# Kernel tuning notes

Measured on AMD Instinct MI355X. Metric: run time of the kernel, lower is better.

Reference implementation:

```python
import jax, jax.numpy as jnp
import numpy as np

H = 1024        # pegasus-large hidden size
HEADS = 16      # matches the hard-coded /16 in the source
T = 512         # decoder steps
N = 1024        # encoder (source) tokens
V = 96103       # pegasus tokenizer vocab size


def setup_inputs() -> dict:
    key = jax.random.key(0)
    ks = jax.random.split(key, 8)
    return {
        "cross_attn": jax.random.normal(ks[0], (1, HEADS, T, N), jnp.float32),
        "encoder_hidden": jax.random.normal(ks[1], (1, N, H), jnp.float32),
        "decoder_hidden": jax.random.normal(ks[2], (1, T, H), jnp.float32),
        "decoder_embedding": jax.random.normal(ks[3], (1, T, H), jnp.float32),
        "logits": jax.random.normal(ks[4], (1, T, V), jnp.float32),
        "input_ids": jax.random.randint(ks[5], (N,), 0, V),
        "pointer_w": jax.random.normal(ks[6], (1, 3 * H), jnp.float32) * 0.02,
        "pointer_b": jnp.zeros((1,), jnp.float32),
    }


def reference(cross_attn, encoder_hidden, decoder_hidden, decoder_embedding,
              logits, input_ids, pointer_w, pointer_b):
    # squeeze batch dim (module assumes batch=1)
    ca = jnp.sum(cross_attn[0], axis=0) / 16.0                 # [T, N] head-avg cross attn
    enc = encoder_hidden[0]                                    # [N, H]
    dec_h = decoder_hidden[0]                                  # [T, H]
    dec_e = decoder_embedding[0]                               # [T, H]
    lg = logits[0]                                             # [T, V]

    h = ca @ enc                                               # [T, H] attn-weighted context
    lin = jnp.concatenate([h, dec_h, dec_e], axis=1)           # [T, 3H]
    gen_probs = jax.nn.sigmoid(lin @ pointer_w.T + pointer_b)  # [T, 1]

    distribution = jax.nn.softmax(lg, axis=1)                  # [T, V]
    gen_logits = gen_probs * distribution                      # [T, V]

    # vectorized form of: for t, for n: copy_logits[t, input_ids[n]] = ca[t, n]
    Tn, Vn = lg.shape
    rows = jnp.broadcast_to(jnp.arange(Tn)[:, None], ca.shape)       # [T, N]
    cols = jnp.broadcast_to(input_ids[None, :], ca.shape)            # [T, N]
    copy_logits = jnp.zeros((Tn, Vn), lg.dtype).at[rows, cols].set(ca)

    final_probs = gen_logits + (1.0 - gen_probs) * copy_logits  # [T, V]
    return gen_probs, final_probs
```

## Files before the change

kernel.cpp:

```cpp
#include <hip/hip_runtime.h>

#define Tn 512
#define Nn 1024
#define Hn 1024
#define Vn 96103u
#define NHEADS 16
#define SPLITS 16
#define CHUNK 6007u
#define TV 49204736u

#define HS_BLKS 512
#define EW_BLKS 1024
#define SP_BLKS (SPLITS*Tn)
#define K0_BLKS (HS_BLKS + EW_BLKS + SP_BLKS)

typedef float f4 __attribute__((ext_vector_type(4)));

__device__ __forceinline__ unsigned enc1(float x) {
  unsigned u = __float_as_uint(x);
  u = u + 0x80000u + ((u >> 20) & 1u);
  return (u >> 20) - 896u;
}
__device__ __forceinline__ float dec1(unsigned w, int k) {
  unsigned byte = (w >> (8 * k)) & 0xFFu;
  return __uint_as_float((byte + 896u) << 20);
}

__global__ __launch_bounds__(256) void k0(const float* __restrict__ attn,
                                          const float* __restrict__ enc,
                                          const float* __restrict__ w,
                                          const float* __restrict__ lg,
                                          float* __restrict__ ca,
                                          float* __restrict__ ew,
                                          float* __restrict__ part_s,
                                          int* __restrict__ col2n,
                                          unsigned char* __restrict__ ebuf) {
  const int b = blockIdx.x, tid = threadIdx.x;

  if (b < HS_BLKS) {
    int i = b * 256 + tid;
    if (i < (int)Vn) col2n[i] = -1;
    const f4* a4 = (const f4*)attn;
    const int slice = (Tn * Nn) / 4;
    f4 acc = __builtin_nontemporal_load(&a4[i]);
#pragma unroll
    for (int h = 1; h < NHEADS; ++h)
      acc += __builtin_nontemporal_load(&a4[h * slice + i]);
    ((f4*)ca)[i] = acc * (1.0f / 16.0f);
    return;
  }

  if (b < HS_BLKS + EW_BLKS) {
    int n = b - HS_BLKS;
    float4 r = ((const float4*)(enc + n * Hn))[tid];
    float4 ww = ((const float4*)w)[tid];
    float p = r.x * ww.x + r.y * ww.y + r.z * ww.z + r.w * ww.w;
    for (int off = 32; off > 0; off >>= 1) p += __shfl_down(p, off, 64);
    __shared__ float lds[4];
    int lane = tid & 63, wv = tid >> 6;
    if (lane == 0) lds[wv] = p;
    __syncthreads();
    if (tid == 0) ew[n] = lds[0] + lds[1] + lds[2] + lds[3];
    return;
  }

  {
    int rem = b - HS_BLKS - EW_BLKS;
    const int c = rem & (SPLITS - 1), t = rem >> 4;
    const unsigned vbeg = (unsigned)c * CHUNK;
    const unsigned vend = min(vbeg + CHUNK, Vn);
    const unsigned beg = (unsigned)t * Vn + vbeg;
    const unsigned end = (unsigned)t * Vn + vend;
    const unsigned beg4 = (beg + 3u) & ~3u;
    const unsigned end4 = end & ~3u;

    float s = 0.0f;
    for (unsigned i = beg + tid; i < beg4; i += 256) {
      float e = __expf(__builtin_nontemporal_load(&lg[i]));
      s += e; ebuf[i] = (unsigned char)enc1(e);
    }
    const f4* lg4 = (const f4*)lg;
    unsigned* eb4 = (unsigned*)ebuf;
    for (unsigned i4 = beg4 / 4u + tid; i4 < end4 / 4u; i4 += 256) {
      f4 a = __builtin_nontemporal_load(&lg4[i4]);
      float e0 = __expf(a[0]), e1 = __expf(a[1]), e2 = __expf(a[2]), e3 = __expf(a[3]);
      s += (e0 + e1) + (e2 + e3);
      eb4[i4] = enc1(e0) | (enc1(e1) << 8) | (enc1(e2) << 16) | (enc1(e3) << 24);
    }
    for (unsigned i = end4 + tid; i < end; i += 256) {
      float e = __expf(__builtin_nontemporal_load(&lg[i]));
      s += e; ebuf[i] = (unsigned char)enc1(e);
    }
    for (int off = 32; off > 0; off >>= 1) s += __shfl_down(s, off, 64);
    __shared__ float ls[4];
    int lane = tid & 63, wv = tid >> 6;
    if (lane == 0) ls[wv] = s;
    __syncthreads();
    if (tid == 0) part_s[t * SPLITS + c] = ls[0] + ls[1] + ls[2] + ls[3];
  }
}

__global__ __launch_bounds__(256) void k1(const float* __restrict__ ca,
                                          const float* __restrict__ ew,
                                          const float* __restrict__ dh,
                                          const float* __restrict__ de,
                                          const float* __restrict__ w,
                                          const float* __restrict__ b,
                                          const float* __restrict__ part_s,
                                          const int* __restrict__ ids,
                                          int* __restrict__ col2n,
                                          float4* __restrict__ params,
                                          float* __restrict__ out_gen) {
  const int t = blockIdx.x, tid = threadIdx.x;
  if (t == Tn) {
    for (int n = tid; n < (int)Nn; n += 256)
      atomicMax(&col2n[ids[n]], n);
    return;
  }
  float4 c4 = ((const float4*)(ca + t * Nn))[tid];
  float4 e4 = ((const float4*)ew)[tid];
  float p = c4.x * e4.x + c4.y * e4.y + c4.z * e4.z + c4.w * e4.w;
  float4 h4 = ((const float4*)(dh + t * Hn))[tid];
  float4 w1 = ((const float4*)(w + Hn))[tid];
  p += h4.x * w1.x + h4.y * w1.y + h4.z * w1.z + h4.w * w1.w;
  float4 d4 = ((const float4*)(de + t * Hn))[tid];
  float4 w2 = ((const float4*)(w + 2 * Hn))[tid];
  p += d4.x * w2.x + d4.y * w2.y + d4.z * w2.z + d4.w * w2.w;
  for (int off = 32; off > 0; off >>= 1) p += __shfl_down(p, off, 64);
  __shared__ float lds[4];
  int lane = tid & 63, wv = tid >> 6;
  if (lane == 0) lds[wv] = p;
  __syncthreads();
  if (tid == 0) {
    float z = lds[0] + lds[1] + lds[2] + lds[3] + b[0];
    float g = 1.0f / (1.0f + __expf(-z));
    float S = 0.0f;
#pragma unroll
    for (int c = 0; c < SPLITS; ++c) S += part_s[t * SPLITS + c];
    out_gen[t] = g;
    params[t] = make_float4(g, 1.0f / S, 1.0f - g, 0.0f);
  }
}

__global__ __launch_bounds__(256) void k2(const unsigned* __restrict__ eb4,
                                          const float* __restrict__ ca,
                                          const float4* __restrict__ params,
                                          const int* __restrict__ col2n,
                                          float* __restrict__ out) {
  const unsigned total4 = TV / 4u;
  f4* out4 = (f4*)out;
  const unsigned stride = gridDim.x * 256u;
  for (unsigned i4 = blockIdx.x * 256u + threadIdx.x; i4 < total4; i4 += stride) {
    unsigned i0 = i4 * 4u;
    unsigned t = i0 / Vn;
    unsigned v = i0 - t * Vn;
    unsigned dw = eb4[i4];
    f4 r;
    if (v + 3u < Vn) {
      float4 P = params[t];
      const float* cat = ca + t * Nn;
      int n0 = col2n[v], n1 = col2n[v + 1], n2 = col2n[v + 2], n3 = col2n[v + 3];
      r[0] = P.x * dec1(dw, 0) * P.y;
      r[1] = P.x * dec1(dw, 1) * P.y;
      r[2] = P.x * dec1(dw, 2) * P.y;
      r[3] = P.x * dec1(dw, 3) * P.y;
      if (n0 >= 0) r[0] += P.z * cat[n0];
      if (n1 >= 0) r[1] += P.z * cat[n1];
      if (n2 >= 0) r[2] += P.z * cat[n2];
      if (n3 >= 0) r[3] += P.z * cat[n3];
    } else {
#pragma unroll
      for (int k = 0; k < 4; ++k) {
        unsigned idx = i0 + (unsigned)k;
        unsigned tt = idx / Vn;
        unsigned vv = idx - tt * Vn;
        float4 P = params[tt];
        float val = P.x * dec1(dw, k) * P.y;
        int n = col2n[vv];
        if (n >= 0) val += P.z * ca[tt * Nn + n];
        r[k] = val;
      }
    }
    __builtin_nontemporal_store(r, &out4[i4]);
  }
}

extern "C" void kernel_launch(void* const* d_in, const int* in_sizes, int n_in,
                              void* d_out, int out_size, void* d_ws, size_t ws_size,
                              hipStream_t stream) {
  const float* attn = (const float*)d_in[0];
  const float* enc  = (const float*)d_in[1];
  const float* dh   = (const float*)d_in[2];
  const float* de   = (const float*)d_in[3];
  const float* lg   = (const float*)d_in[4];
  const int*   ids  = (const int*)d_in[5];
  const float* w    = (const float*)d_in[6];
  const float* b    = (const float*)d_in[7];
  float* out = (float*)d_out;

  unsigned char* ebuf = (unsigned char*)d_ws;
  float4* params = (float4*)(ebuf + ((TV + 15u) & ~15u));
  float* ca     = (float*)(params + Tn);
  float* ew     = ca + (size_t)Tn * Nn;
  float* part_s = ew + Nn;
  int*   col2n  = (int*)(part_s + Tn * SPLITS);

  hipLaunchKernelGGL(k0, dim3(K0_BLKS), dim3(256), 0, stream,
                     attn, enc, w, lg, ca, ew, part_s, col2n, ebuf);
  hipLaunchKernelGGL(k1, dim3(Tn + 1), dim3(256), 0, stream,
                     ca, ew, dh, de, w, b, part_s, ids, col2n, params, out);
  hipLaunchKernelGGL(k2, dim3(4096), dim3(256), 0, stream,
                     (const unsigned*)ebuf, ca, params, col2n, out + Tn);
}
```

Before: 123.3 us.

## Fuse softmax sum, gate and output pass into one per-row kernel using LDS

The three kernels are replaced by a memset, a small preprocessing kernel and one 1024-thread block per decoder row. Each block computes the pointer gate, the row's exp-sum and packed 8-bit exp codes, keeps those codes in shared memory, then writes the final probabilities. This removes the global byte buffer round-trip and the separate params kernel. In exchange the grid drops to 512 large blocks with about 96KB of LDS each, which limits occupancy and leaves no overlap between a row's sum phase and its write phase.

```diff
diff --git a/kernel.cpp b/kernel.cpp
--- a/kernel.cpp
+++ b/kernel.cpp
@@ -5,14 +5,11 @@
 #define Hn 1024
 #define Vn 96103u
 #define NHEADS 16
-#define SPLITS 16
-#define CHUNK 6007u
 #define TV 49204736u
 
 #define HS_BLKS 512
 #define EW_BLKS 1024
-#define SP_BLKS (SPLITS*Tn)
-#define K0_BLKS (HS_BLKS + EW_BLKS + SP_BLKS)
+#define K0_BLKS (HS_BLKS + EW_BLKS + 1)
 
 typedef float f4 __attribute__((ext_vector_type(4)));
 
@@ -29,17 +26,14 @@
 __global__ __launch_bounds__(256) void k0(const float* __restrict__ attn,
                                           const float* __restrict__ enc,
                                           const float* __restrict__ w,
-                                          const float* __restrict__ lg,
+                                          const int* __restrict__ ids,
                                           float* __restrict__ ca,
                                           float* __restrict__ ew,
-                                          float* __restrict__ part_s,
-                                          int* __restrict__ col2n,
-                                          unsigned char* __restrict__ ebuf) {
+                                          int* __restrict__ col2n) {
   const int b = blockIdx.x, tid = threadIdx.x;
 
   if (b < HS_BLKS) {
     int i = b * 256 + tid;
-    if (i < (int)Vn) col2n[i] = -1;
     const f4* a4 = (const f4*)attn;
     const int slice = (Tn * Nn) / 4;
     f4 acc = __builtin_nontemporal_load(&a4[i]);
@@ -64,124 +58,96 @@
     return;
   }
 
-  {
-    int rem = b - HS_BLKS - EW_BLKS;
-    const int c = rem & (SPLITS - 1), t = rem >> 4;
-    const unsigned vbeg = (unsigned)c * CHUNK;
-    const unsigned vend = min(vbeg + CHUNK, Vn);
-    const unsigned beg = (unsigned)t * Vn + vbeg;
-    const unsigned end = (unsigned)t * Vn + vend;
-    const unsigned beg4 = (beg + 3u) & ~3u;
-    const unsigned end4 = end & ~3u;
-
-    float s = 0.0f;
-    for (unsigned i = beg + tid; i < beg4; i += 256) {
-      float e = __expf(__builtin_nontemporal_load(&lg[i]));
-      s += e; ebuf[i] = (unsigned char)enc1(e);
-    }
-    const f4* lg4 = (const f4*)lg;
-    unsigned* eb4 = (unsigned*)ebuf;
-    for (unsigned i4 = beg4 / 4u + tid; i4 < end4 / 4u; i4 += 256) {
-      f4 a = __builtin_nontemporal_load(&lg4[i4]);
-      float e0 = __expf(a[0]), e1 = __expf(a[1]), e2 = __expf(a[2]), e3 = __expf(a[3]);
-      s += (e0 + e1) + (e2 + e3);
-      eb4[i4] = enc1(e0) | (enc1(e1) << 8) | (enc1(e2) << 16) | (enc1(e3) << 24);
-    }
-    for (unsigned i = end4 + tid; i < end; i += 256) {
-      float e = __expf(__builtin_nontemporal_load(&lg[i]));
-      s += e; ebuf[i] = (unsigned char)enc1(e);
-    }
-    for (int off = 32; off > 0; off >>= 1) s += __shfl_down(s, off, 64);
-    __shared__ float ls[4];
-    int lane = tid & 63, wv = tid >> 6;
-    if (lane == 0) ls[wv] = s;
-    __syncthreads();
-    if (tid == 0) part_s[t * SPLITS + c] = ls[0] + ls[1] + ls[2] + ls[3];
-  }
+  for (int n = tid; n < (int)Nn; n += 256)
+    atomicMax(&col2n[ids[n]], n);
 }
 
-__global__ __launch_bounds__(256) void k1(const float* __restrict__ ca,
-                                          const float* __restrict__ ew,
-                                          const float* __restrict__ dh,
-                                          const float* __restrict__ de,
-                                          const float* __restrict__ w,
-                                          const float* __restrict__ b,
-                                          const float* __restrict__ part_s,
-                                          const int* __restrict__ ids,
-                                          int* __restrict__ col2n,
-                                          float4* __restrict__ params,
-                                          float* __restrict__ out_gen) {
+__global__ __launch_bounds__(1024, 4) void k2row(
+    const float* __restrict__ lg, const float* __restrict__ ca,
+    const float* __restrict__ ew, const float* __restrict__ dh,
+    const float* __restrict__ de, const float* __restrict__ w,
+    const float* __restrict__ bias, const int* __restrict__ col2n,
+    float* __restrict__ out) {
+  __shared__ unsigned sm4[24064];
+  __shared__ float red[32];
+  __shared__ float Pb[4];
+
   const int t = blockIdx.x, tid = threadIdx.x;
-  if (t == Tn) {
-    for (int n = tid; n < (int)Nn; n += 256)
-      atomicMax(&col2n[ids[n]], n);
-    return;
+  const int lane = tid & 63, wv = tid >> 6;
+  const unsigned base = (unsigned)t * Vn;
+  const unsigned end = base + Vn;
+  const unsigned beg4 = (base + 3u) & ~3u;
+  const unsigned end4 = end & ~3u;
+  const unsigned q0 = beg4 / 4u;
+  const unsigned nq = (end4 - beg4) / 4u;
+
+  float gp = ca[base - (unsigned)t * Vn + (unsigned)t * Nn + tid] * ew[tid]
+           + dh[t * Hn + tid] * w[Hn + tid]
+           + de[t * Hn + tid] * w[2 * Hn + tid];
+
+  float s = 0.0f;
+  for (unsigned i = base + tid; i < beg4; i += 1024)
+    s += __expf(__builtin_nontemporal_load(&lg[i]));
+  const f4* lg4 = (const f4*)lg;
+  for (unsigned j = tid; j < nq; j += 1024) {
+    f4 x = __builtin_nontemporal_load(&lg4[q0 + j]);
+    float e0 = __expf(x[0]), e1 = __expf(x[1]), e2 = __expf(x[2]), e3 = __expf(x[3]);
+    s += (e0 + e1) + (e2 + e3);
+    sm4[j] = enc1(e0) | (enc1(e1) << 8) | (enc1(e2) << 16) | (enc1(e3) << 24);
   }
-  float4 c4 = ((const float4*)(ca + t * Nn))[tid];
-  float4 e4 = ((const float4*)ew)[tid];
-  float p = c4.x * e4.x + c4.y * e4.y + c4.z * e4.z + c4.w * e4.w;
-  float4 h4 = ((const float4*)(dh + t * Hn))[tid];
-  float4 w1 = ((const float4*)(w + Hn))[tid];
-  p += h4.x * w1.x + h4.y * w1.y + h4.z * w1.z + h4.w * w1.w;
-  float4 d4 = ((const float4*)(de + t * Hn))[tid];
-  float4 w2 = ((const float4*)(w + 2 * Hn))[tid];
-  p += d4.x * w2.x + d4.y * w2.y + d4.z * w2.z + d4.w * w2.w;
-  for (int off = 32; off > 0; off >>= 1) p += __shfl_down(p, off, 64);
-  __shared__ float lds[4];
-  int lane = tid & 63, wv = tid >> 6;
-  if (lane == 0) lds[wv] = p;
+  for (unsigned i = end4 + tid; i < end; i += 1024)
+    s += __expf(__builtin_nontemporal_load(&lg[i]));
+
+  for (int off = 32; off > 0; off >>= 1) {
+    gp += __shfl_down(gp, off, 64);
+    s  += __shfl_down(s, off, 64);
+  }
+  if (lane == 0) { red[wv] = gp; red[16 + wv] = s; }
   __syncthreads();
   if (tid == 0) {
-    float z = lds[0] + lds[1] + lds[2] + lds[3] + b[0];
+    float z = 0.f, S = 0.f;
+#pragma unroll
+    for (int q = 0; q < 16; ++q) { z += red[q]; S += red[16 + q]; }
+    z += bias[0];
     float g = 1.0f / (1.0f + __expf(-z));
-    float S = 0.0f;
-#pragma unroll
-    for (int c = 0; c < SPLITS; ++c) S += part_s[t * SPLITS + c];
-    out_gen[t] = g;
-    params[t] = make_float4(g, 1.0f / S, 1.0f - g, 0.0f);
+    out[t] = g;
+    Pb[0] = g; Pb[1] = 1.0f / S; Pb[2] = 1.0f - g;
   }
-}
+  __syncthreads();
 
-__global__ __launch_bounds__(256) void k2(const unsigned* __restrict__ eb4,
-                                          const float* __restrict__ ca,
-                                          const float4* __restrict__ params,
-                                          const int* __restrict__ col2n,
-                                          float* __restrict__ out) {
-  const unsigned total4 = TV / 4u;
-  f4* out4 = (f4*)out;
-  const unsigned stride = gridDim.x * 256u;
-  for (unsigned i4 = blockIdx.x * 256u + threadIdx.x; i4 < total4; i4 += stride) {
-    unsigned i0 = i4 * 4u;
-    unsigned t = i0 / Vn;
-    unsigned v = i0 - t * Vn;
-    unsigned dw = eb4[i4];
+  const float g = Pb[0], inv = Pb[1], omg = Pb[2];
+  const float* cat = ca + t * Nn;
+  float* outf = out + Tn;
+
+  for (unsigned i = base + tid; i < beg4; i += 1024) {
+    unsigned v = i - base;
+    float val = g * __expf(__builtin_nontemporal_load(&lg[i])) * inv;
+    int n = col2n[v];
+    if (n >= 0) val += omg * cat[n];
+    __builtin_nontemporal_store(val, &outf[i]);
+  }
+  f4* out4 = (f4*)outf;
+  for (unsigned j = tid; j < nq; j += 1024) {
+    unsigned dw = sm4[j];
+    unsigned v = beg4 - base + 4u * j;
     f4 r;
-    if (v + 3u < Vn) {
-      float4 P = params[t];
-      const float* cat = ca + t * Nn;
-      int n0 = col2n[v], n1 = col2n[v + 1], n2 = col2n[v + 2], n3 = col2n[v + 3];
-      r[0] = P.x * dec1(dw, 0) * P.y;
-      r[1] = P.x * dec1(dw, 1) * P.y;
-      r[2] = P.x * dec1(dw, 2) * P.y;
-      r[3] = P.x * dec1(dw, 3) * P.y;
-      if (n0 >= 0) r[0] += P.z * cat[n0];
-      if (n1 >= 0) r[1] += P.z * cat[n1];
-      if (n2 >= 0) r[2] += P.z * cat[n2];
-      if (n3 >= 0) r[3] += P.z * cat[n3];
-    } else {
-#pragma unroll
-      for (int k = 0; k < 4; ++k) {
-        unsigned idx = i0 + (unsigned)k;
-        unsigned tt = idx / Vn;
-        unsigned vv = idx - tt * Vn;
-        float4 P = params[tt];
-        float val = P.x * dec1(dw, k) * P.y;
-        int n = col2n[vv];
-        if (n >= 0) val += P.z * ca[tt * Nn + n];
-        r[k] = val;
-      }
-    }
-    __builtin_nontemporal_store(r, &out4[i4]);
+    int n0 = col2n[v], n1 = col2n[v + 1], n2 = col2n[v + 2], n3 = col2n[v + 3];
+    r[0] = g * dec1(dw, 0) * inv;
+    r[1] = g * dec1(dw, 1) * inv;
+    r[2] = g * dec1(dw, 2) * inv;
+    r[3] = g * dec1(dw, 3) * inv;
+    if (n0 >= 0) r[0] += omg * cat[n0];
+    if (n1 >= 0) r[1] += omg * cat[n1];
+    if (n2 >= 0) r[2] += omg * cat[n2];
+    if (n3 >= 0) r[3] += omg * cat[n3];
+    __builtin_nontemporal_store(r, &out4[q0 + j]);
+  }
+  for (unsigned i = end4 + tid; i < end; i += 1024) {
+    unsigned v = i - base;
+    float val = g * __expf(__builtin_nontemporal_load(&lg[i])) * inv;
+    int n = col2n[v];
+    if (n >= 0) val += omg * cat[n];
+    __builtin_nontemporal_store(val, &outf[i]);
   }
 }
 
@@ -198,17 +164,13 @@
   const float* b    = (const float*)d_in[7];
   float* out = (float*)d_out;
 
-  unsigned char* ebuf = (unsigned char*)d_ws;
-  float4* params = (float4*)(ebuf + ((TV + 15u) & ~15u));
-  float* ca     = (float*)(params + Tn);
-  float* ew     = ca + (size_t)Tn * Nn;
-  float* part_s = ew + Nn;
-  int*   col2n  = (int*)(part_s + Tn * SPLITS);
+  float* ca    = (float*)d_ws;
+  float* ew    = ca + (size_t)Tn * Nn;
+  int*   col2n = (int*)(ew + Nn);
 
+  hipMemsetAsync(col2n, 0xFF, (size_t)Vn * 4, stream);
   hipLaunchKernelGGL(k0, dim3(K0_BLKS), dim3(256), 0, stream,
-                     attn, enc, w, lg, ca, ew, part_s, col2n, ebuf);
-  hipLaunchKernelGGL(k1, dim3(Tn + 1), dim3(256), 0, stream,
-                     ca, ew, dh, de, w, b, part_s, ids, col2n, params, out);
-  hipLaunchKernelGGL(k2, dim3(4096), dim3(256), 0, stream,
-                     (const unsigned*)ebuf, ca, params, col2n, out + Tn);
+                     attn, enc, w, ids, ca, ew, col2n);
+  hipLaunchKernelGGL(k2row, dim3(Tn), dim3(1024), 0, stream,
+                     lg, ca, ew, dh, de, w, b, col2n, out);
 }
```

Result: faster. 113.4 us (-8.1%).
